# Optimization experiments

Measured on AMD Instinct MI355X. Metric: run time of the kernel, lower is better.

Reference implementation:

```python
import jax, jax.numpy as jnp
import numpy as np

BEV_FEAT_SHAPE = (1, 1, 200, 200, 64)  # (B, Dz, Dy, Dx, C)
MAXN = 40

B, N, D, IH, IW = 1, 6, 118, 16, 44
C = 64
N_RANKS = BEV_FEAT_SHAPE[1] * BEV_FEAT_SHAPE[2] * BEV_FEAT_SHAPE[3] * MAXN


def setup_inputs() -> dict:
    key = jax.random.key(0)
    k1, k2, k3, k4 = jax.random.split(key, 4)
    depth = jax.random.uniform(k1, (B, N, D, IH, IW), dtype=jnp.float32)
    feat = jax.random.normal(k2, (B, N, IH, IW, C), dtype=jnp.float32)
    # indices may point at the appended zero row (index == total rows)
    ranks_depth = jax.random.randint(k3, (N_RANKS,), 0, B * N * D * IH * IW + 1, dtype=jnp.int32)
    ranks_feat = jax.random.randint(k4, (N_RANKS,), 0, B * N * IH * IW + 1, dtype=jnp.int32)
    return {"depth": depth, "feat": feat, "ranks_depth": ranks_depth,
            "ranks_feat": ranks_feat, "maxn": MAXN}


def reference(depth, feat, ranks_depth, ranks_feat, maxn):
    b, n, d, ih, iw = depth.shape
    c = feat.shape[-1]
    _, oD, oW, oH, _ = BEV_FEAT_SHAPE
    # flatten + append one zero padding row (invalid points map here)
    depth_2d = jnp.concatenate(
        [depth.reshape(b * n * d * ih * iw, 1), jnp.zeros((1, 1), jnp.float32)], axis=0)
    feat_2d = jnp.concatenate(
        [feat.reshape(b * n * ih * iw, c), jnp.zeros((1, c), jnp.float32)], axis=0)
    # gather depth scalar and feature vector per point, multiply
    r_mul = depth_2d[ranks_depth] * feat_2d[ranks_feat]  # (oD*oW*oH*maxn, C)
    # segmented sum: maxn points per output voxel
    r_scatter = r_mul.reshape(oD, oW, oH, maxn, c).sum(axis=3, keepdims=True)
    # permute (oD, oW, oH, 1, C) -> (1, oD, oW, oH, C)
    return jnp.transpose(r_scatter, (3, 0, 1, 2, 4))
```

## Files before the change

kernel.cpp:

```cpp
#include <hip/hip_runtime.h>


typedef int      vint4   __attribute__((ext_vector_type(4)));
typedef float    vfloat4 __attribute__((ext_vector_type(4)));
typedef _Float16 vhalf4  __attribute__((ext_vector_type(4)));

#define ND_ROWS (1 * 6 * 118 * 16 * 44)
#define NF_ROWS (1 * 6 * 16 * 44)
#define MAXN_PTS 40
#define NVOX (200 * 200)
#define VOX_PER_BLOCK 16
#define PAIR4_PER_BLOCK (VOX_PER_BLOCK * MAXN_PTS / 4)
#define LDS_STRIDE 41

#define FEAT_VEC4 (NF_ROWS * 16)

__global__ __launch_bounds__(256) void feat_pack_f16(
    const vfloat4* __restrict__ in, vhalf4* __restrict__ out)
{
    const int i = blockIdx.x * 256 + threadIdx.x;
    const vfloat4 f = in[i];
    vhalf4 h;
    h.x = (_Float16)f.x; h.y = (_Float16)f.y;
    h.z = (_Float16)f.z; h.w = (_Float16)f.w;
    out[i] = h;
}

__global__ __launch_bounds__(256) void BEVPoolV2_79783312491037_kernel(
    const float* __restrict__ depth,
    const vhalf4* __restrict__ feat16,
    const vint4* __restrict__ rd4,
    const vint4* __restrict__ rf4,
    vfloat4* __restrict__ out4)
{
    __shared__ float2 s_pair[VOX_PER_BLOCK * LDS_STRIDE];

    const int t = threadIdx.x;

    if (t < PAIR4_PER_BLOCK) {
        const vint4 rd = __builtin_nontemporal_load(&rd4[blockIdx.x * PAIR4_PER_BLOCK + t]);
        const vint4 rf = __builtin_nontemporal_load(&rf4[blockIdx.x * PAIR4_PER_BLOCK + t]);
        const int base = t * 4;
#pragma unroll
        for (int k = 0; k < 4; ++k) {
            const int idx = base + k;
            const int g = idx / MAXN_PTS;
            const int j = idx - g * MAXN_PTS;
            const int rdk = rd[k], rfk = rf[k];
            const bool valid = (rdk < ND_ROWS) && (rfk < NF_ROWS);
            const float dl = depth[min(rdk, ND_ROWS - 1)];
            float2 p;
            p.x = valid ? dl : 0.0f;
            p.y = __int_as_float((rfk < NF_ROWS) ? rfk : 0);
            s_pair[g * LDS_STRIDE + j] = p;
        }
    }
    __syncthreads();

    const int g = t >> 4;
    const int c4 = t & 15;
    const int pbase = g * LDS_STRIDE;

    vfloat4 acc = {0.0f, 0.0f, 0.0f, 0.0f};
#pragma unroll
    for (int j = 0; j < MAXN_PTS; ++j) {
        const float2 p = s_pair[pbase + j];
        const float d = p.x;
        const int rf = __float_as_int(p.y);
        const vhalf4 f = feat16[rf * 16 + c4];
        acc.x = fmaf(d, (float)f.x, acc.x);
        acc.y = fmaf(d, (float)f.y, acc.y);
        acc.z = fmaf(d, (float)f.z, acc.z);
        acc.w = fmaf(d, (float)f.w, acc.w);
    }

    __builtin_nontemporal_store(acc, &out4[blockIdx.x * 256 + t]);
}

extern "C" void kernel_launch(void* const* d_in, const int* in_sizes, int n_in,
                              void* d_out, int out_size, void* d_ws, size_t ws_size,
                              hipStream_t stream)
{
    const float*   depth  = (const float*)d_in[0];
    const vfloat4* feat4  = (const vfloat4*)d_in[1];
    const vint4*   rd4    = (const vint4*)d_in[2];
    const vint4*   rf4    = (const vint4*)d_in[3];
    vfloat4* out4 = (vfloat4*)d_out;

    vhalf4* feat16 = (vhalf4*)d_ws;

    feat_pack_f16<<<FEAT_VEC4 / 256, 256, 0, stream>>>(feat4, feat16);

    const int blocks = NVOX / VOX_PER_BLOCK;
    BEVPoolV2_79783312491037_kernel<<<blocks, 256, 0, stream>>>(
        depth, feat16, rd4, rf4, out4);
}
```

Before: 94.62 us.

## Widen feature gathers to 16 bytes with double-buffered prefetch and 128-thread blocks

After: 92.04 us. -2.7%, faster.

```diff
diff --git a/kernel.cpp b/kernel.cpp
--- a/kernel.cpp
+++ b/kernel.cpp
@@ -4,14 +4,17 @@
 typedef int      vint4   __attribute__((ext_vector_type(4)));
 typedef float    vfloat4 __attribute__((ext_vector_type(4)));
 typedef _Float16 vhalf4  __attribute__((ext_vector_type(4)));
+typedef _Float16 vhalf8  __attribute__((ext_vector_type(8)));
 
 #define ND_ROWS (1 * 6 * 118 * 16 * 44)
 #define NF_ROWS (1 * 6 * 16 * 44)
 #define MAXN_PTS 40
 #define NVOX (200 * 200)
-#define VOX_PER_BLOCK 16
-#define PAIR4_PER_BLOCK (VOX_PER_BLOCK * MAXN_PTS / 4)
+#define VPB 16
+#define THREADS 128
+#define CHUNKS (VPB * MAXN_PTS / 4)
 #define LDS_STRIDE 41
+#define ROW_BYTES 128
 
 #define FEAT_VEC4 (NF_ROWS * 16)
 
@@ -26,72 +29,100 @@
     out[i] = h;
 }
 
-__global__ __launch_bounds__(256) void BEVPoolV2_79783312491037_kernel(
+__global__ __launch_bounds__(THREADS) void BEVPoolV2_79783312491037_kernel(
     const float* __restrict__ depth,
     const vhalf4* __restrict__ feat16,
     const vint4* __restrict__ rd4,
     const vint4* __restrict__ rf4,
     vfloat4* __restrict__ out4)
 {
-    __shared__ float2 s_pair[VOX_PER_BLOCK * LDS_STRIDE];
+    __shared__ float2 s_pair[VPB * LDS_STRIDE];
 
     const int t = threadIdx.x;
 
-    if (t < PAIR4_PER_BLOCK) {
-        const vint4 rd = __builtin_nontemporal_load(&rd4[blockIdx.x * PAIR4_PER_BLOCK + t]);
-        const vint4 rf = __builtin_nontemporal_load(&rf4[blockIdx.x * PAIR4_PER_BLOCK + t]);
-        const int base = t * 4;
 #pragma unroll
-        for (int k = 0; k < 4; ++k) {
-            const int idx = base + k;
-            const int g = idx / MAXN_PTS;
-            const int j = idx - g * MAXN_PTS;
-            const int rdk = rd[k], rfk = rf[k];
-            const bool valid = (rdk < ND_ROWS) && (rfk < NF_ROWS);
-            const float dl = depth[min(rdk, ND_ROWS - 1)];
-            float2 p;
-            p.x = valid ? dl : 0.0f;
-            p.y = __int_as_float((rfk < NF_ROWS) ? rfk : 0);
-            s_pair[g * LDS_STRIDE + j] = p;
+    for (int r = 0; r < 2; ++r) {
+        const int c = r * THREADS + t;
+        if (c < CHUNKS) {
+            const vint4 rd = __builtin_nontemporal_load(&rd4[blockIdx.x * CHUNKS + c]);
+            const vint4 rf = __builtin_nontemporal_load(&rf4[blockIdx.x * CHUNKS + c]);
+#pragma unroll
+            for (int k = 0; k < 4; ++k) {
+                const int idx = c * 4 + k;
+                const int g = idx / MAXN_PTS;
+                const int j = idx - g * MAXN_PTS;
+                const int rdk = rd[k], rfk = rf[k];
+                const bool valid = (rdk < ND_ROWS) && (rfk < NF_ROWS);
+                const float dl = depth[min(rdk, ND_ROWS - 1)];
+                float2 p;
+                p.x = valid ? dl : 0.0f;
+                p.y = __uint_as_float((unsigned)((rfk < NF_ROWS) ? rfk : 0) * ROW_BYTES);
+                s_pair[g * LDS_STRIDE + j] = p;
+            }
         }
     }
     __syncthreads();
 
-    const int g = t >> 4;
-    const int c4 = t & 15;
+    const int g = t >> 3;
+    const int c8 = t & 7;
     const int pbase = g * LDS_STRIDE;
+    const char* fbase = (const char*)feat16 + c8 * 16;
 
-    vfloat4 acc = {0.0f, 0.0f, 0.0f, 0.0f};
+    float acc[8] = {0, 0, 0, 0, 0, 0, 0, 0};
+
+    float  db[2][8];
+    vhalf8 fb[2][8];
+
 #pragma unroll
-    for (int j = 0; j < MAXN_PTS; ++j) {
-        const float2 p = s_pair[pbase + j];
-        const float d = p.x;
-        const int rf = __float_as_int(p.y);
-        const vhalf4 f = feat16[rf * 16 + c4];
-        acc.x = fmaf(d, (float)f.x, acc.x);
-        acc.y = fmaf(d, (float)f.y, acc.y);
-        acc.z = fmaf(d, (float)f.z, acc.z);
-        acc.w = fmaf(d, (float)f.w, acc.w);
+    for (int k = 0; k < 8; ++k) {
+        const float2 p = s_pair[pbase + k];
+        db[0][k] = p.x;
+        fb[0][k] = *(const vhalf8*)(fbase + __float_as_uint(p.y));
     }
 
-    __builtin_nontemporal_store(acc, &out4[blockIdx.x * 256 + t]);
+#pragma unroll
+    for (int b = 0; b < 5; ++b) {
+        const int cur = b & 1, nxt = cur ^ 1;
+        if (b < 4) {
+#pragma unroll
+            for (int k = 0; k < 8; ++k) {
+                const float2 p = s_pair[pbase + (b + 1) * 8 + k];
+                db[nxt][k] = p.x;
+                fb[nxt][k] = *(const vhalf8*)(fbase + __float_as_uint(p.y));
+            }
+        }
+#pragma unroll
+        for (int k = 0; k < 8; ++k) {
+            const float d = db[cur][k];
+            const vhalf8 f = fb[cur][k];
+#pragma unroll
+            for (int i = 0; i < 8; ++i)
+                acc[i] = fmaf(d, (float)f[i], acc[i]);
+        }
+    }
+
+    const int v = blockIdx.x * VPB + g;
+    vfloat4 lo = {acc[0], acc[1], acc[2], acc[3]};
+    vfloat4 hi = {acc[4], acc[5], acc[6], acc[7]};
+    __builtin_nontemporal_store(lo, &out4[v * 16 + c8 * 2]);
+    __builtin_nontemporal_store(hi, &out4[v * 16 + c8 * 2 + 1]);
 }
 
 extern "C" void kernel_launch(void* const* d_in, const int* in_sizes, int n_in,
                               void* d_out, int out_size, void* d_ws, size_t ws_size,
                               hipStream_t stream)
 {
-    const float*   depth  = (const float*)d_in[0];
-    const vfloat4* feat4  = (const vfloat4*)d_in[1];
-    const vint4*   rd4    = (const vint4*)d_in[2];
-    const vint4*   rf4    = (const vint4*)d_in[3];
+    const float*   depth = (const float*)d_in[0];
+    const vfloat4* feat4 = (const vfloat4*)d_in[1];
+    const vint4*   rd4   = (const vint4*)d_in[2];
+    const vint4*   rf4   = (const vint4*)d_in[3];
     vfloat4* out4 = (vfloat4*)d_out;
 
     vhalf4* feat16 = (vhalf4*)d_ws;
 
     feat_pack_f16<<<FEAT_VEC4 / 256, 256, 0, stream>>>(feat4, feat16);
 
-    const int blocks = NVOX / VOX_PER_BLOCK;
-    BEVPoolV2_79783312491037_kernel<<<blocks, 256, 0, stream>>>(
+    const int blocks = NVOX / VPB;
+    BEVPoolV2_79783312491037_kernel<<<blocks, THREADS, 0, stream>>>(
         depth, feat16, rd4, rf4, out4);
 }
```
